# Performance work log

Measured on AMD Instinct MI355X. Metric: run time of the kernel, lower is better.

Reference implementation:

```python
import jax, jax.numpy as jnp
import numpy as np
import math

LIMBS = [(5, 7), (7, 9), (6, 8), (8, 10), (11, 13), (13, 15), (12, 14), (14, 16), (5, 6), (11, 12), (5, 11), (6, 12), (5, 12), (6, 11)]
PARENT = jnp.array([l[0] for l in LIMBS], dtype=jnp.int32)
CHILD = jnp.array([l[1] for l in LIMBS], dtype=jnp.int32)
EXPECTED_2D_LEN = 0.15

B = 65536
D_MODEL = 64
HID = 128


def _ln(x, g, b, eps=1e-5):
    m = jnp.mean(x, axis=-1, keepdims=True)
    v = jnp.mean(jnp.square(x - m), axis=-1, keepdims=True)
    return (x - m) * jax.lax.rsqrt(v + eps) * g + b


def _unit(x, eps=1e-6):
    # F.normalize semantics: divide by max(norm, eps)
    n = jnp.linalg.norm(x, axis=-1, keepdims=True)
    return x / jnp.maximum(n, eps)


def setup_inputs() -> dict:
    key = jax.random.key(0)
    ks = jax.random.split(key, 32)
    d = {}
    d["joint_features"] = jax.random.normal(ks[0], (B, 17, D_MODEL), jnp.float32)
    d["pose_2d"] = jax.random.normal(ks[1], (B, 17, 2), jnp.float32)
    d["pose_3d"] = jax.random.normal(ks[2], (B, 17, 3), jnp.float32)
    d["azimuth"] = jax.random.uniform(ks[3], (B,), jnp.float32) * 360.0
    d["elevation"] = jax.random.uniform(ks[4], (B,), jnp.float32) * 180.0 - 90.0
    d["projected_2d"] = jax.random.normal(ks[5], (B, 17, 2), jnp.float32)

    def lin(k, out_f, in_f, std=None):
        s = std if std is not None else 1.0 / math.sqrt(in_f)
        return jax.random.normal(k, (out_f, in_f), jnp.float32) * s

    # current_orient_encoder: Linear(3->32), LayerNorm(32), ReLU
    d["co_w"] = lin(ks[6], HID // 4, 3)
    d["co_b"] = jnp.zeros((HID // 4,), jnp.float32)
    d["co_g"] = jnp.ones((HID // 4,), jnp.float32)
    d["co_be"] = jnp.zeros((HID // 4,), jnp.float32)
    # limb_2d_encoder: Linear(4->64), LayerNorm(64), ReLU
    d["l2_w"] = lin(ks[7], HID // 2, 4)
    d["l2_b"] = jnp.zeros((HID // 2,), jnp.float32)
    d["l2_g"] = jnp.ones((HID // 2,), jnp.float32)
    d["l2_be"] = jnp.zeros((HID // 2,), jnp.float32)
    # view_encoder: Linear(7->32), ReLU
    d["v_w"] = lin(ks[8], HID // 4, 7)
    d["v_b"] = jnp.zeros((HID // 4,), jnp.float32)
    # limb_head: Linear(256->128), LN(128), LeakyReLU, Linear(128->128), LeakyReLU, Linear(128->3)
    in_dim = HID // 2 + HID // 4 + D_MODEL * 2 + HID // 4  # 256
    d["h1_w"] = lin(ks[9], HID, in_dim)
    d["h1_b"] = jnp.zeros((HID,), jnp.float32)
    d["h_g"] = jnp.ones((HID,), jnp.float32)
    d["h_be"] = jnp.zeros((HID,), jnp.float32)
    d["h2_w"] = lin(ks[10], HID, HID)
    d["h2_b"] = jnp.zeros((HID,), jnp.float32)
    d["h3_w"] = lin(ks[11], 3, HID, std=0.01)
    d["h3_b"] = jnp.zeros((3,), jnp.float32)
    return d


def reference(joint_features, pose_2d, pose_3d, azimuth, elevation, projected_2d,
              co_w, co_b, co_g, co_be, l2_w, l2_b, l2_g, l2_be, v_w, v_b,
              h1_w, h1_b, h_g, h_be, h2_w, h2_b, h3_w, h3_b):
    nl = PARENT.shape[0]  # 14
    # gather parent/child joint features: (B, 14, d_model)
    pf = joint_features[:, PARENT, :]
    cf = joint_features[:, CHILD, :]
    # current 3D orientations from input pose
    cur = _unit(pose_3d[:, CHILD, :] - pose_3d[:, PARENT, :])  # (B,14,3)
    co = jax.nn.relu(_ln(jnp.einsum('blk,ok->blo', cur, co_w) + co_b, co_g, co_be))
    # view encoder from azimuth/elevation
    az = azimuth * (math.pi / 180.0)
    el = elevation * (math.pi / 180.0)
    sa, ca, se, ce = jnp.sin(az), jnp.cos(az), jnp.sin(el), jnp.cos(el)
    view_in = jnp.stack([sa * ce, se, ca * ce, sa, ca, se, ce], axis=-1)  # (B,7)
    vf = jax.nn.relu(view_in @ v_w.T + v_b)  # (B,32)
    vf = jnp.broadcast_to(vf[:, None, :], (vf.shape[0], nl, vf.shape[-1]))
    # 2D foreshortening features from projected_2d
    v2 = projected_2d[:, CHILD, :] - projected_2d[:, PARENT, :]  # (B,14,2)
    L = jnp.linalg.norm(v2, axis=-1, keepdims=True)
    d2 = v2 / (L + 1e-6)
    ratio = L / (EXPECTED_2D_LEN + 1e-6)
    feat2d = jnp.concatenate([d2, L, ratio], axis=-1)  # (B,14,4)
    l2 = jax.nn.relu(_ln(jnp.einsum('blk,ok->blo', feat2d, l2_w) + l2_b, l2_g, l2_be))
    # concat all branches: (B,14,256)
    lf = jnp.concatenate([l2, co, pf, cf, vf], axis=-1)
    # 3-layer MLP head
    h = jax.nn.leaky_relu(_ln(jnp.einsum('blk,ok->blo', lf, h1_w) + h1_b, h_g, h_be), 0.2)
    h = jax.nn.leaky_relu(jnp.einsum('blk,ok->blo', h, h2_w) + h2_b, 0.2)
    delta = jnp.einsum('blk,ok->blo', h, h3_w) + h3_b  # (B,14,3)
    return _unit(cur + delta)
```

## Files before the change

kernel.cpp:

```cpp
#include <hip/hip_runtime.h>


#define NTHR   1024
#define NBLK   256
#define NTILES 14336
#define NROWS  917504
#define C2D    6.66662222251852f
#define RAD    0.017453292519943295f
#define WS_STAT_OFF 98304
#define WS_SCAL_OFF 131072

typedef __bf16 bf16x8 __attribute__((ext_vector_type(8)));
typedef __bf16 bf16x4 __attribute__((ext_vector_type(4)));
typedef float  f32x4  __attribute__((ext_vector_type(4)));

#define PARENT_PK 0x10106097863120ull
#define CHILD_PK  0x677671b9a85342ull

__global__ __launch_bounds__(256) void prep_kernel(
    const float* __restrict__ w1, const float* __restrict__ w2,
    __bf16* __restrict__ wsb)
{
  const int u = blockIdx.x * 256 + threadIdx.x;
  if (u < 4096) {
    const int lane = u & 63, t = u >> 6;
    const int f = t & 1, kk = (t >> 1) & 7, wn = t >> 4;
    const int col = wn * 32 + f * 16 + (lane & 15);
    const int kb  = kk * 32 + (lane >> 4) * 8;
    __bf16* dst = wsb + (size_t)u * 8;
    #pragma unroll
    for (int j = 0; j < 8; ++j) dst[j] = (__bf16)w1[col * 256 + kb + j];
  } else if (u < 6144) {
    const int v = u - 4096;
    const int lane = v & 63, t = v >> 6;
    const int f = t & 1, kk = (t >> 1) & 3, wn = t >> 3;
    const int col = wn * 32 + f * 16 + (lane & 15);
    const int kb  = kk * 32 + (lane >> 4) * 8;
    __bf16* dst = wsb + 32768 + (size_t)v * 8;
    #pragma unroll
    for (int j = 0; j < 8; ++j) dst[j] = (__bf16)w2[col * 128 + kb + j];
  }
}

__global__ __launch_bounds__(64) void prep0_kernel(
    const float* __restrict__ cow, const float* __restrict__ cob,
    const float* __restrict__ l2w, const float* __restrict__ l2b,
    float* __restrict__ statg)
{
  const int o = threadIdx.x;
  const float w0 = l2w[o * 4 + 0], w1v = l2w[o * 4 + 1];
  const float w2v = l2w[o * 4 + 2] + C2D * l2w[o * 4 + 3];
  const float bo = l2b[o];
  float v[14] = { w0, w1v, w2v, bo, w0 * w0, w0 * w1v, w0 * w2v,
                  w1v * w1v, w1v * w2v, w2v * w2v, w0 * bo, w1v * bo, w2v * bo, bo * bo };
  float c0 = 0.f, c1 = 0.f, c2 = 0.f, cb = 0.f;
  if (o < 32) { c0 = cow[o * 3 + 0]; c1 = cow[o * 3 + 1]; c2 = cow[o * 3 + 2]; cb = cob[o]; }
  float u[14] = { c0, c1, c2, cb, c0 * c0, c0 * c1, c0 * c2,
                  c1 * c1, c1 * c2, c2 * c2, c0 * cb, c1 * cb, c2 * cb, cb * cb };
  #pragma unroll
  for (int k = 0; k < 14; ++k) {
    #pragma unroll
    for (int m = 1; m < 64; m <<= 1) { v[k] += __shfl_xor(v[k], m, 64); u[k] += __shfl_xor(u[k], m, 64); }
  }
  if (o == 0) {
    const float i64 = 1.f / 64.f, i32 = 1.f / 32.f;
    const float lmx = v[0] * i64, lmy = v[1] * i64, lmz = v[2] * i64, lmb = v[3] * i64;
    statg[0] = lmx; statg[1] = lmy; statg[2] = lmz; statg[3] = lmb;
    statg[4] = v[4] * i64 - lmx * lmx;        statg[5] = 2.f * (v[5] * i64 - lmx * lmy);
    statg[6] = 2.f * (v[6] * i64 - lmx * lmz); statg[7] = v[7] * i64 - lmy * lmy;
    statg[8] = 2.f * (v[8] * i64 - lmy * lmz); statg[9] = v[9] * i64 - lmz * lmz;
    statg[10] = 2.f * (v[10] * i64 - lmx * lmb); statg[11] = 2.f * (v[11] * i64 - lmy * lmb);
    statg[12] = 2.f * (v[12] * i64 - lmz * lmb); statg[13] = v[13] * i64 - lmb * lmb;
    const float cmx = u[0] * i32, cmy = u[1] * i32, cmz = u[2] * i32, cmb = u[3] * i32;
    statg[14] = cmx; statg[15] = cmy; statg[16] = cmz; statg[17] = cmb;
    statg[18] = u[4] * i32 - cmx * cmx;        statg[19] = 2.f * (u[5] * i32 - cmx * cmy);
    statg[20] = 2.f * (u[6] * i32 - cmx * cmz); statg[21] = u[7] * i32 - cmy * cmy;
    statg[22] = 2.f * (u[8] * i32 - cmy * cmz); statg[23] = u[9] * i32 - cmz * cmz;
    statg[24] = 2.f * (u[10] * i32 - cmx * cmb); statg[25] = 2.f * (u[11] * i32 - cmy * cmb);
    statg[26] = 2.f * (u[12] * i32 - cmz * cmb); statg[27] = u[13] * i32 - cmb * cmb;
  }
}

__global__ __launch_bounds__(256) void prep2_kernel(
    const float* __restrict__ p3g, const float* __restrict__ az,
    const float* __restrict__ el,  const float* __restrict__ p2d,
    const float* __restrict__ statg, f32x4* __restrict__ scalg)
{
  const int r = blockIdx.x * 256 + threadIdx.x;
  const unsigned rg = (unsigned)r;
  const unsigned b = rg / 14u;
  const int l = (int)(rg - b * 14u);
  const int p = 5 + (int)((PARENT_PK >> (4 * l)) & 15ull);
  const int c = 5 + (int)((CHILD_PK  >> (4 * l)) & 15ull);
  const float* p3 = p3g + (size_t)b * 51;
  const float dx = p3[c * 3 + 0] - p3[p * 3 + 0];
  const float dy = p3[c * 3 + 1] - p3[p * 3 + 1];
  const float dz = p3[c * 3 + 2] - p3[p * 3 + 2];
  const float* q2 = p2d + (size_t)b * 34;
  const float vx = q2[c * 2 + 0] - q2[p * 2 + 0];
  const float vy = q2[c * 2 + 1] - q2[p * 2 + 1];
  const float sazv = az[b], selv = el[b];

  const float ci = 1.f / fmaxf(sqrtf(dx * dx + dy * dy + dz * dz), 1e-6f);
  const float cx = dx * ci, cy = dy * ci, cz = dz * ci;
  const float L  = sqrtf(vx * vx + vy * vy);
  const float il = 1.f / (L + 1e-6f);
  const float f0 = vx * il, f1 = vy * il;
  const float azr = sazv * RAD, elr = selv * RAD;
  const float sa = __sinf(azr), ca = __cosf(azr);
  const float se = __sinf(elr), ce = __cosf(elr);
  const float vl = statg[4] * f0 * f0 + statg[7] * f1 * f1 + statg[9] * L * L +
                   statg[5] * f0 * f1 + statg[6] * f0 * L + statg[8] * f1 * L +
                   statg[10] * f0 + statg[11] * f1 + statg[12] * L + statg[13];
  const float vc = statg[18] * cx * cx + statg[21] * cy * cy + statg[23] * cz * cz +
                   statg[19] * cx * cy + statg[20] * cx * cz + statg[22] * cy * cz +
                   statg[24] * cx + statg[25] * cy + statg[26] * cz + statg[27];
  f32x4 s0; s0[0] = cx; s0[1] = cy; s0[2] = cz; s0[3] = f0;
  f32x4 s1; s1[0] = f1; s1[1] = L; s1[2] = rsqrtf(vl + 1e-5f); s1[3] = rsqrtf(vc + 1e-5f);
  f32x4 s2; s2[0] = sa * ce; s2[1] = se; s2[2] = ca * ce; s2[3] = sa;
  f32x4 s3; s3[0] = ca; s3[1] = ce; s3[2] = 0.f; s3[3] = 0.f;
  scalg[(size_t)r * 4 + 0] = s0; scalg[(size_t)r * 4 + 1] = s1;
  scalg[(size_t)r * 4 + 2] = s2; scalg[(size_t)r * 4 + 3] = s3;
}

struct Smem {
  __bf16 w1f[32768];
  __bf16 w2f[16384];
  __bf16 lf[64][264];
  __bf16 h [64][132];
  f32x4  scal4[256];
  float  w3c[384];
  float  h1b[128], hg[128], hbe[128], h2b[128];
  float  partG1[512];
  float  partG2[768];
};

__device__ __forceinline__ float RFL(float x) {
  return __uint_as_float((unsigned)__builtin_amdgcn_readfirstlane((int)__float_as_uint(x)));
}

template<bool PRECOMP>
__global__ __launch_bounds__(NTHR, 4) void limb_kernel(
    const float* __restrict__ jf,  const float* __restrict__ p3g,
    const float* __restrict__ az,  const float* __restrict__ el,
    const float* __restrict__ p2d,
    const float* __restrict__ cow, const float* __restrict__ cob,
    const float* __restrict__ cog, const float* __restrict__ cobe,
    const float* __restrict__ l2w, const float* __restrict__ l2b,
    const float* __restrict__ l2g, const float* __restrict__ l2be,
    const float* __restrict__ vw,  const float* __restrict__ vb,
    const float* __restrict__ h1bg, const float* __restrict__ hgg,
    const float* __restrict__ hbeg, const float* __restrict__ h2bg,
    const float* __restrict__ w3,  const float* __restrict__ h3bg,
    const __bf16* __restrict__ wsb, const f32x4* __restrict__ scalg,
    float* __restrict__ out)
{
  __shared__ Smem sm;
  const int tid  = threadIdx.x;
  const int wave = tid >> 6;
  const int lane = tid & 63;
  const int lrow = lane & 15, lk8 = lane >> 4;
  const int mp = wave >> 2, nt = wave & 3;
  const int nrow = nt * 16 + lrow;
  const int cb0 = mp * 32 + lk8 * 4;
  const int cb1 = cb0 + 16;
  const int myrow0 = wave * 4;

  {
    const uint4* s1 = (const uint4*)wsb;
    uint4* d1 = (uint4*)sm.w1f;
    for (int i = tid; i < 4096; i += NTHR) d1[i] = s1[i];
    const uint4* s2 = (const uint4*)(wsb + 32768);
    uint4* d2 = (uint4*)sm.w2f;
    for (int i = tid; i < 2048; i += NTHR) d2[i] = s2[i];
  }
  if (tid < 384) sm.w3c[tid] = w3[tid];
  if (tid < 128) {
    sm.h1b[tid] = h1bg[tid]; sm.hg[tid] = hgg[tid];
    sm.hbe[tid] = hbeg[tid]; sm.h2b[tid] = h2bg[tid];
  }
  const float h3b0 = h3bg[0], h3b1 = h3bg[1], h3b2 = h3bg[2];

  float lQxx, lQxy2, lQxz2, lQyy, lQyz2, lQzz, lrx2, lry2, lrz2, ls0;
  float lmx, lmy, lmz, lmb;
  {
    float s1x = 0, s1y = 0, s1z = 0, sb = 0;
    float sxx = 0, sxy = 0, sxz = 0, syy = 0, syz = 0, szz = 0;
    float sbx = 0, sby = 0, sbz = 0, sbb = 0;
    for (int o = 0; o < 64; ++o) {
      const float w0 = l2w[o * 4 + 0], w1v = l2w[o * 4 + 1];
      const float w2v = l2w[o * 4 + 2] + C2D * l2w[o * 4 + 3];
      const float bo = l2b[o];
      s1x += w0; s1y += w1v; s1z += w2v; sb += bo;
      sxx += w0 * w0; sxy += w0 * w1v; sxz += w0 * w2v;
      syy += w1v * w1v; syz += w1v * w2v; szz += w2v * w2v;
      sbx += w0 * bo; sby += w1v * bo; sbz += w2v * bo; sbb += bo * bo;
    }
    const float i = 1.f / 64.f;
    lmx = RFL(s1x * i); lmy = RFL(s1y * i); lmz = RFL(s1z * i); lmb = RFL(sb * i);
    lQxx = RFL(sxx * i - lmx * lmx); lQxy2 = RFL(2.f * (sxy * i - lmx * lmy));
    lQxz2 = RFL(2.f * (sxz * i - lmx * lmz)); lQyy = RFL(syy * i - lmy * lmy);
    lQyz2 = RFL(2.f * (syz * i - lmy * lmz)); lQzz = RFL(szz * i - lmz * lmz);
    lrx2 = RFL(2.f * (sbx * i - lmx * lmb)); lry2 = RFL(2.f * (sby * i - lmy * lmb));
    lrz2 = RFL(2.f * (sbz * i - lmz * lmb)); ls0 = RFL(sbb * i - lmb * lmb);
  }
  float cQxx, cQxy2, cQxz2, cQyy, cQyz2, cQzz, crx2, cry2, crz2, cs0;
  float cmx, cmy, cmz, cmb;
  {
    float s1x = 0, s1y = 0, s1z = 0, sb = 0;
    float sxx = 0, sxy = 0, sxz = 0, syy = 0, syz = 0, szz = 0;
    float sbx = 0, sby = 0, sbz = 0, sbb = 0;
    for (int o = 0; o < 32; ++o) {
      const float w0 = cow[o * 3 + 0], w1v = cow[o * 3 + 1], w2v = cow[o * 3 + 2];
      const float bo = cob[o];
      s1x += w0; s1y += w1v; s1z += w2v; sb += bo;
      sxx += w0 * w0; sxy += w0 * w1v; sxz += w0 * w2v;
      syy += w1v * w1v; syz += w1v * w2v; szz += w2v * w2v;
      sbx += w0 * bo; sby += w1v * bo; sbz += w2v * bo; sbb += bo * bo;
    }
    const float i = 1.f / 32.f;
    cmx = RFL(s1x * i); cmy = RFL(s1y * i); cmz = RFL(s1z * i); cmb = RFL(sb * i);
    cQxx = RFL(sxx * i - cmx * cmx); cQxy2 = RFL(2.f * (sxy * i - cmx * cmy));
    cQxz2 = RFL(2.f * (sxz * i - cmx * cmz)); cQyy = RFL(syy * i - cmy * cmy);
    cQyz2 = RFL(2.f * (syz * i - cmy * cmz)); cQzz = RFL(szz * i - cmz * cmz);
    crx2 = RFL(2.f * (sbx * i - cmx * cmb)); cry2 = RFL(2.f * (sby * i - cmy * cmb));
    crz2 = RFL(2.f * (sbz * i - cmz * cmb)); cs0 = RFL(sbb * i - cmb * cmb);
  }

  const float lwc0 = l2w[lane * 4 + 0] - lmx;
  const float lwc1 = l2w[lane * 4 + 1] - lmy;
  const float lwc2 = (l2w[lane * 4 + 2] + C2D * l2w[lane * 4 + 3]) - lmz;
  const float lbc  = l2b[lane] - lmb;
  const float lgv  = l2g[lane], lbev = l2be[lane];
  float u0, u1, u2, u3, u4, u5, u6;
  if (lane < 32) {
    u0 = cow[lane * 3 + 0] - cmx; u1 = cow[lane * 3 + 1] - cmy;
    u2 = cow[lane * 3 + 2] - cmz; u3 = cob[lane] - cmb;
    u4 = cog[lane]; u5 = cobe[lane]; u6 = 0.f;
  } else {
    const int o = lane - 32;
    u0 = vw[o * 7 + 0]; u1 = vw[o * 7 + 1] + vw[o * 7 + 5];
    u2 = vw[o * 7 + 2]; u3 = vw[o * 7 + 3];
    u4 = vw[o * 7 + 4]; u5 = vw[o * 7 + 6]; u6 = vb[o];
  }

  auto jf_src = [&](int rg0x, int round) -> const float* {
    const int task = wave * 8 + round * 4 + lk8;
    const int row = task >> 1, half = task & 1;
    const unsigned rg = (unsigned)(rg0x + row);
    const unsigned b = rg / 14u;
    const int l = (int)(rg - b * 14u);
    const int j = half ? 5 + (int)((CHILD_PK >> (4 * l)) & 15ull)
                       : 5 + (int)((PARENT_PK >> (4 * l)) & 15ull);
    return jf + ((size_t)b * 17 + (size_t)j) * 64 + lrow * 4;
  };
  auto jf_store = [&](int round, float4 v) {
    const int task = wave * 8 + round * 4 + lk8;
    const int row = task >> 1, half = task & 1;
    bf16x4 o; o[0] = (__bf16)v.x; o[1] = (__bf16)v.y; o[2] = (__bf16)v.z; o[3] = (__bf16)v.w;
    *(bf16x4*)&sm.lf[row][(half ? 160 : 96) + lrow * 4] = o;
  };
  struct G12 { float p3p0, p3p1, p3p2, p3c0, p3c1, p3c2, q2p0, q2p1, q2c0, q2c1, sazv, selv; };
  auto gather12_row = [&](int rgl) -> G12 {
    G12 g;
    const unsigned rg = (unsigned)rgl;
    const unsigned b = rg / 14u;
    const int l = (int)(rg - b * 14u);
    const int p = 5 + (int)((PARENT_PK >> (4 * l)) & 15ull);
    const int c = 5 + (int)((CHILD_PK  >> (4 * l)) & 15ull);
    const float* p3 = p3g + (size_t)b * 51;
    g.p3p0 = p3[p * 3 + 0]; g.p3p1 = p3[p * 3 + 1]; g.p3p2 = p3[p * 3 + 2];
    g.p3c0 = p3[c * 3 + 0]; g.p3c1 = p3[c * 3 + 1]; g.p3c2 = p3[c * 3 + 2];
    const float* q2 = p2d + (size_t)b * 34;
    g.q2p0 = q2[p * 2 + 0]; g.q2p1 = q2[p * 2 + 1];
    g.q2c0 = q2[c * 2 + 0]; g.q2c1 = q2[c * 2 + 1];
    g.sazv = az[b]; g.selv = el[b];
    return g;
  };
  auto scal_write = [&](int row, const G12& g) {
    const float dx = g.p3c0 - g.p3p0, dy = g.p3c1 - g.p3p1, dz = g.p3c2 - g.p3p2;
    const float ci = 1.f / fmaxf(sqrtf(dx * dx + dy * dy + dz * dz), 1e-6f);
    const float cx = dx * ci, cy = dy * ci, cz = dz * ci;
    const float vx = g.q2c0 - g.q2p0, vy = g.q2c1 - g.q2p1;
    const float L  = sqrtf(vx * vx + vy * vy);
    const float il = 1.f / (L + 1e-6f);
    const float f0 = vx * il, f1 = vy * il;
    const float azr = g.sazv * RAD, elr = g.selv * RAD;
    const float sa = __sinf(azr), ca = __cosf(azr);
    const float se = __sinf(elr), ce = __cosf(elr);
    const float vl = lQxx * f0 * f0 + lQyy * f1 * f1 + lQzz * L * L +
                     lQxy2 * f0 * f1 + lQxz2 * f0 * L + lQyz2 * f1 * L +
                     lrx2 * f0 + lry2 * f1 + lrz2 * L + ls0;
    const float vc = cQxx * cx * cx + cQyy * cy * cy + cQzz * cz * cz +
                     cQxy2 * cx * cy + cQxz2 * cx * cz + cQyz2 * cy * cz +
                     crx2 * cx + cry2 * cy + crz2 * cz + cs0;
    f32x4 s0; s0[0] = cx; s0[1] = cy; s0[2] = cz; s0[3] = f0;
    f32x4 s1; s1[0] = f1; s1[1] = L; s1[2] = rsqrtf(vl + 1e-5f); s1[3] = rsqrtf(vc + 1e-5f);
    f32x4 s2; s2[0] = sa * ce; s2[1] = se; s2[2] = ca * ce; s2[3] = sa;
    f32x4 s3; s3[0] = ca; s3[1] = ce; s3[2] = 0.f; s3[3] = 0.f;
    sm.scal4[row * 4 + 0] = s0; sm.scal4[row * 4 + 1] = s1;
    sm.scal4[row * 4 + 2] = s2; sm.scal4[row * 4 + 3] = s3;
  };
  auto expandB = [&]() {
    #pragma unroll
    for (int rr = 0; rr < 4; ++rr) {
      const int row = myrow0 + rr;
      const f32x4 s0 = sm.scal4[row * 4 + 0];
      const f32x4 s1 = sm.scal4[row * 4 + 1];
      const f32x4 s2 = sm.scal4[row * 4 + 2];
      const f32x4 s3 = sm.scal4[row * 4 + 3];
      {
        const float a = lwc0 * s0[3] + lwc1 * s1[0] + lwc2 * s1[1] + lbc;
        sm.lf[row][lane] = (__bf16)fmaxf(a * s1[2] * lgv + lbev, 0.f);
      }
      if (lane < 32) {
        const float a = u0 * s0[0] + u1 * s0[1] + u2 * s0[2] + u3;
        sm.lf[row][64 + lane] = (__bf16)fmaxf(a * s1[3] * u4 + u5, 0.f);
      } else {
        const float a = u0 * s2[0] + u1 * s2[1] + u2 * s2[2] + u3 * s2[3] +
                        u4 * s3[0] + u5 * s3[1] + u6;
        sm.lf[row][224 + (lane - 32)] = (__bf16)fmaxf(a, 0.f);
      }
    }
  };

  {
    const int rg0 = blockIdx.x * 64;
    jf_store(0, *(const float4*)jf_src(rg0, 0));
    jf_store(1, *(const float4*)jf_src(rg0, 1));
    if (lane < 4) {
      if (PRECOMP) {
        const f32x4* sp = scalg + (size_t)(rg0 + myrow0 + lane) * 4;
        sm.scal4[(myrow0 + lane) * 4 + 0] = sp[0];
        sm.scal4[(myrow0 + lane) * 4 + 1] = sp[1];
        sm.scal4[(myrow0 + lane) * 4 + 2] = sp[2];
        sm.scal4[(myrow0 + lane) * 4 + 3] = sp[3];
      } else {
        scal_write(myrow0 + lane, gather12_row(rg0 + myrow0 + lane));
      }
    }
    expandB();
  }
  __syncthreads();

  float curx = 0.f, cury = 0.f, curz = 0.f;
  int prevT = -1;

  for (int tile = blockIdx.x; tile < NTILES; tile += NBLK) {
    const int ntile = tile + NBLK;
    const bool pv = ntile < NTILES;

    float4 jva = {0.f, 0.f, 0.f, 0.f}, jvb = jva;
    f32x4 s0n = {0.f, 0.f, 0.f, 0.f}, s1n = s0n, s2n = s0n, s3n = s0n;
    G12 g = {};
    if (pv) {
      jva = *(const float4*)jf_src(ntile * 64, 0);
      jvb = *(const float4*)jf_src(ntile * 64, 1);
      if (lane < 4) {
        if (PRECOMP) {
          const f32x4* sp = scalg + (size_t)(ntile * 64 + myrow0 + lane) * 4;
          s0n = sp[0]; s1n = sp[1]; s2n = sp[2]; s3n = sp[3];
        } else {
          g = gather12_row(ntile * 64 + myrow0 + lane);
        }
      }
    }
    if (prevT >= 0 && lane < 4) {
      const int r = myrow0 + lane;
      const f32x4 q0 = *(const f32x4*)&sm.partG2[r * 12];
      const f32x4 q1 = *(const f32x4*)&sm.partG2[r * 12 + 4];
      const f32x4 q2 = *(const f32x4*)&sm.partG2[r * 12 + 8];
      const float ox = curx + q0[0] + q0[1] + q0[2] + q0[3] + h3b0;
      const float oy = cury + q1[0] + q1[1] + q1[2] + q1[3] + h3b1;
      const float oz = curz + q2[0] + q2[1] + q2[2] + q2[3] + h3b2;
      const float nn = sqrtf(ox * ox + oy * oy + oz * oz);
      const float iv = 1.f / fmaxf(nn, 1e-6f);
      const size_t o0 = (size_t)(prevT * 64 + r) * 3;
      out[o0 + 0] = ox * iv; out[o0 + 1] = oy * iv; out[o0 + 2] = oz * iv;
    }
    f32x4 a0 = {0.f, 0.f, 0.f, 0.f}, a1 = a0;
    #pragma unroll
    for (int kk = 0; kk < 8; ++kk) {
      const bf16x8 fb  = *(const bf16x8*)&sm.lf[nrow][kk * 32 + lk8 * 8];
      const bf16x8 fa0 = *(const bf16x8*)&sm.w1f[(((mp * 8 + kk) * 2 + 0) * 64 + lane) * 8];
      const bf16x8 fa1 = *(const bf16x8*)&sm.w1f[(((mp * 8 + kk) * 2 + 1) * 64 + lane) * 8];
      a0 = __builtin_amdgcn_mfma_f32_16x16x32_bf16(fa0, fb, a0, 0, 0, 0);
      a1 = __builtin_amdgcn_mfma_f32_16x16x32_bf16(fa1, fb, a1, 0, 0, 0);
    }
    const f32x4 hb0 = *(const f32x4*)&sm.h1b[cb0];
    const f32x4 hb1 = *(const f32x4*)&sm.h1b[cb1];
    float v0[4], v1[4], ss = 0.f, qq = 0.f;
    #pragma unroll
    for (int j = 0; j < 4; ++j) {
      v0[j] = a0[j] + hb0[j]; v1[j] = a1[j] + hb1[j];
      ss += v0[j] + v1[j];
      qq = fmaf(v0[j], v0[j], qq); qq = fmaf(v1[j], v1[j], qq);
    }
    ss += __shfl_xor(ss, 16, 64); ss += __shfl_xor(ss, 32, 64);
    qq += __shfl_xor(qq, 16, 64); qq += __shfl_xor(qq, 32, 64);
    if (lk8 == 0) *(float2*)&sm.partG1[nrow * 8 + mp * 2] = make_float2(ss, qq);
    __syncthreads();

    {
      const f32x4 pa = *(const f32x4*)&sm.partG1[nrow * 8];
      const f32x4 pb = *(const f32x4*)&sm.partG1[nrow * 8 + 4];
      const float mean = (pa[0] + pa[2] + pb[0] + pb[2]) * (1.f / 128.f);
      const float var  = (pa[1] + pa[3] + pb[1] + pb[3]) * (1.f / 128.f) - mean * mean;
      const float rs = rsqrtf(var + 1e-5f);
      const f32x4 g0 = *(const f32x4*)&sm.hg[cb0],  g1 = *(const f32x4*)&sm.hg[cb1];
      const f32x4 e0 = *(const f32x4*)&sm.hbe[cb0], e1 = *(const f32x4*)&sm.hbe[cb1];
      bf16x4 y0, y1;
      #pragma unroll
      for (int j = 0; j < 4; ++j) {
        float t0 = (v0[j] - mean) * rs * g0[j] + e0[j]; t0 = (t0 > 0.f) ? t0 : 0.2f * t0;
        float t1 = (v1[j] - mean) * rs * g1[j] + e1[j]; t1 = (t1 > 0.f) ? t1 : 0.2f * t1;
        y0[j] = (__bf16)t0; y1[j] = (__bf16)t1;
      }
      *(bf16x4*)&sm.h[nrow][cb0] = y0;
      *(bf16x4*)&sm.h[nrow][cb1] = y1;
    }
    __syncthreads();

    f32x4 d0 = {0.f, 0.f, 0.f, 0.f}, d1 = d0;
    #pragma unroll
    for (int kk = 0; kk < 4; ++kk) {
      const bf16x8 fbh = *(const bf16x8*)&sm.h[nrow][kk * 32 + lk8 * 8];
      const bf16x8 fa0 = *(const bf16x8*)&sm.w2f[(((mp * 4 + kk) * 2 + 0) * 64 + lane) * 8];
      const bf16x8 fa1 = *(const bf16x8*)&sm.w2f[(((mp * 4 + kk) * 2 + 1) * 64 + lane) * 8];
      d0 = __builtin_amdgcn_mfma_f32_16x16x32_bf16(fa0, fbh, d0, 0, 0, 0);
      d1 = __builtin_amdgcn_mfma_f32_16x16x32_bf16(fa1, fbh, d1, 0, 0, 0);
    }
    if (pv) { jf_store(0, jva); jf_store(1, jvb); }
    if (lane < 4) {
      const f32x4 cu = sm.scal4[(myrow0 + lane) * 4];
      curx = cu[0]; cury = cu[1]; curz = cu[2];
      if (pv) {
        if (PRECOMP) {
          sm.scal4[(myrow0 + lane) * 4 + 0] = s0n;
          sm.scal4[(myrow0 + lane) * 4 + 1] = s1n;
          sm.scal4[(myrow0 + lane) * 4 + 2] = s2n;
          sm.scal4[(myrow0 + lane) * 4 + 3] = s3n;
        } else {
          scal_write(myrow0 + lane, g);
        }
      }
    }
    {
      const f32x4 b20 = *(const f32x4*)&sm.h2b[cb0], b21 = *(const f32x4*)&sm.h2b[cb1];
      const f32x4 wx0 = *(const f32x4*)&sm.w3c[cb0],        wx1 = *(const f32x4*)&sm.w3c[cb1];
      const f32x4 wy0 = *(const f32x4*)&sm.w3c[128 + cb0],  wy1 = *(const f32x4*)&sm.w3c[128 + cb1];
      const f32x4 wz0 = *(const f32x4*)&sm.w3c[256 + cb0],  wz1 = *(const f32x4*)&sm.w3c[256 + cb1];
      float p0 = 0.f, p1 = 0.f, p2 = 0.f;
      #pragma unroll
      for (int j = 0; j < 4; ++j) {
        float x0 = d0[j] + b20[j]; x0 = (x0 > 0.f) ? x0 : 0.2f * x0;
        float x1 = d1[j] + b21[j]; x1 = (x1 > 0.f) ? x1 : 0.2f * x1;
        p0 = fmaf(x0, wx0[j], fmaf(x1, wx1[j], p0));
        p1 = fmaf(x0, wy0[j], fmaf(x1, wy1[j], p1));
        p2 = fmaf(x0, wz0[j], fmaf(x1, wz1[j], p2));
      }
      p0 += __shfl_xor(p0, 16, 64); p0 += __shfl_xor(p0, 32, 64);
      p1 += __shfl_xor(p1, 16, 64); p1 += __shfl_xor(p1, 32, 64);
      p2 += __shfl_xor(p2, 16, 64); p2 += __shfl_xor(p2, 32, 64);
      if (lk8 == 0) {
        sm.partG2[nrow * 12 + 0 + mp] = p0;
        sm.partG2[nrow * 12 + 4 + mp] = p1;
        sm.partG2[nrow * 12 + 8 + mp] = p2;
      }
    }
    if (pv) expandB();
    __syncthreads();
    prevT = tile;
  }

  if (lane < 4) {
    const int r = myrow0 + lane;
    const f32x4 q0 = *(const f32x4*)&sm.partG2[r * 12];
    const f32x4 q1 = *(const f32x4*)&sm.partG2[r * 12 + 4];
    const f32x4 q2 = *(const f32x4*)&sm.partG2[r * 12 + 8];
    const float ox = curx + q0[0] + q0[1] + q0[2] + q0[3] + h3b0;
    const float oy = cury + q1[0] + q1[1] + q1[2] + q1[3] + h3b1;
    const float oz = curz + q2[0] + q2[1] + q2[2] + q2[3] + h3b2;
    const float nn = sqrtf(ox * ox + oy * oy + oz * oz);
    const float iv = 1.f / fmaxf(nn, 1e-6f);
    const size_t o0 = (size_t)(prevT * 64 + r) * 3;
    out[o0 + 0] = ox * iv; out[o0 + 1] = oy * iv; out[o0 + 2] = oz * iv;
  }
}

extern "C" void kernel_launch(void* const* d_in, const int* in_sizes, int n_in,
                              void* d_out, int out_size, void* d_ws, size_t ws_size,
                              hipStream_t stream) {
  (void)in_sizes; (void)n_in; (void)out_size;
  const float* jf   = (const float*)d_in[0];
  const float* p3   = (const float*)d_in[2];
  const float* az   = (const float*)d_in[3];
  const float* el   = (const float*)d_in[4];
  const float* p2d  = (const float*)d_in[5];
  const float* cow  = (const float*)d_in[6];
  const float* cob  = (const float*)d_in[7];
  const float* cog  = (const float*)d_in[8];
  const float* cobe = (const float*)d_in[9];
  const float* l2w  = (const float*)d_in[10];
  const float* l2b  = (const float*)d_in[11];
  const float* l2g  = (const float*)d_in[12];
  const float* l2be = (const float*)d_in[13];
  const float* vw   = (const float*)d_in[14];
  const float* vb   = (const float*)d_in[15];
  const float* w1   = (const float*)d_in[16];
  const float* h1b  = (const float*)d_in[17];
  const float* hg   = (const float*)d_in[18];
  const float* hbe  = (const float*)d_in[19];
  const float* w2   = (const float*)d_in[20];
  const float* h2b  = (const float*)d_in[21];
  const float* w3   = (const float*)d_in[22];
  const float* h3b  = (const float*)d_in[23];

  __bf16* wsb   = (__bf16*)d_ws;
  float*  statg = (float*)((char*)d_ws + WS_STAT_OFF);
  f32x4*  scalg = (f32x4*)((char*)d_ws + WS_SCAL_OFF);

  const size_t ws_need = (size_t)WS_SCAL_OFF + (size_t)NROWS * 64;
  const bool pre = ws_size >= ws_need;

  prep_kernel<<<dim3(24), dim3(256), 0, stream>>>(w1, w2, wsb);
  if (pre) {
    prep0_kernel<<<dim3(1), dim3(64), 0, stream>>>(cow, cob, l2w, l2b, statg);
    prep2_kernel<<<dim3(NROWS / 256), dim3(256), 0, stream>>>(p3, az, el, p2d, statg, scalg);
    limb_kernel<true><<<dim3(NBLK), dim3(NTHR), 0, stream>>>(
        jf, p3, az, el, p2d, cow, cob, cog, cobe,
        l2w, l2b, l2g, l2be, vw, vb,
        h1b, hg, hbe, h2b, w3, h3b, wsb, scalg, (float*)d_out);
  } else {
    limb_kernel<false><<<dim3(NBLK), dim3(NTHR), 0, stream>>>(
        jf, p3, az, el, p2d, cow, cob, cog, cobe,
        l2w, l2b, l2g, l2be, vw, vb,
        h1b, hg, hbe, h2b, w3, h3b, wsb, scalg, (float*)d_out);
  }
}
```

Baseline: 316.5 us.

## Software-pipeline MLP layers across tiles to drop one barrier per tile

Restructures the persistent tile loop into a two-stage software pipeline. Each iteration runs layer 2 and 3 on the previous tile's hidden activations while running layer 1 and the LayerNorm statistics on the current tile. This removes one __syncthreads per tile and lets the two GEMM phases interleave. The cost is an extra prologue/epilogue iteration, conditional branches, and more live registers, and the reuse of sm.h and partG2 across iterations must be ordered correctly.

```diff
diff --git a/kernel.cpp b/kernel.cpp
--- a/kernel.cpp
+++ b/kernel.cpp
@@ -4,6 +4,7 @@
 #define NTHR   1024
 #define NBLK   256
 #define NTILES 14336
+#define NIT    56
 #define NROWS  917504
 #define C2D    6.66662222251852f
 #define RAD    0.017453292519943295f
@@ -344,16 +345,18 @@
   __syncthreads();
 
   float curx = 0.f, cury = 0.f, curz = 0.f;
-  int prevT = -1;
-
-  for (int tile = blockIdx.x; tile < NTILES; tile += NBLK) {
-    const int ntile = tile + NBLK;
-    const bool pv = ntile < NTILES;
+
+  for (int it = 0; it <= NIT; ++it) {
+    const int tile  = blockIdx.x + it * NBLK;
+    const bool hasG1 = it < NIT;
+    const bool hasG2 = it > 0;
+    const bool pv    = (it + 1) < NIT;
 
     float4 jva = {0.f, 0.f, 0.f, 0.f}, jvb = jva;
     f32x4 s0n = {0.f, 0.f, 0.f, 0.f}, s1n = s0n, s2n = s0n, s3n = s0n;
     G12 g = {};
     if (pv) {
+      const int ntile = tile + NBLK;
       jva = *(const float4*)jf_src(ntile * 64, 0);
       jvb = *(const float4*)jf_src(ntile * 64, 1);
       if (lane < 4) {
@@ -365,43 +368,65 @@
         }
       }
     }
-    if (prevT >= 0 && lane < 4) {
-      const int r = myrow0 + lane;
-      const f32x4 q0 = *(const f32x4*)&sm.partG2[r * 12];
-      const f32x4 q1 = *(const f32x4*)&sm.partG2[r * 12 + 4];
-      const f32x4 q2 = *(const f32x4*)&sm.partG2[r * 12 + 8];
-      const float ox = curx + q0[0] + q0[1] + q0[2] + q0[3] + h3b0;
-      const float oy = cury + q1[0] + q1[1] + q1[2] + q1[3] + h3b1;
-      const float oz = curz + q2[0] + q2[1] + q2[2] + q2[3] + h3b2;
-      const float nn = sqrtf(ox * ox + oy * oy + oz * oz);
-      const float iv = 1.f / fmaxf(nn, 1e-6f);
-      const size_t o0 = (size_t)(prevT * 64 + r) * 3;
-      out[o0 + 0] = ox * iv; out[o0 + 1] = oy * iv; out[o0 + 2] = oz * iv;
-    }
-    f32x4 a0 = {0.f, 0.f, 0.f, 0.f}, a1 = a0;
-    #pragma unroll
-    for (int kk = 0; kk < 8; ++kk) {
-      const bf16x8 fb  = *(const bf16x8*)&sm.lf[nrow][kk * 32 + lk8 * 8];
-      const bf16x8 fa0 = *(const bf16x8*)&sm.w1f[(((mp * 8 + kk) * 2 + 0) * 64 + lane) * 8];
-      const bf16x8 fa1 = *(const bf16x8*)&sm.w1f[(((mp * 8 + kk) * 2 + 1) * 64 + lane) * 8];
-      a0 = __builtin_amdgcn_mfma_f32_16x16x32_bf16(fa0, fb, a0, 0, 0, 0);
-      a1 = __builtin_amdgcn_mfma_f32_16x16x32_bf16(fa1, fb, a1, 0, 0, 0);
-    }
-    const f32x4 hb0 = *(const f32x4*)&sm.h1b[cb0];
-    const f32x4 hb1 = *(const f32x4*)&sm.h1b[cb1];
-    float v0[4], v1[4], ss = 0.f, qq = 0.f;
-    #pragma unroll
-    for (int j = 0; j < 4; ++j) {
-      v0[j] = a0[j] + hb0[j]; v1[j] = a1[j] + hb1[j];
-      ss += v0[j] + v1[j];
-      qq = fmaf(v0[j], v0[j], qq); qq = fmaf(v1[j], v1[j], qq);
-    }
-    ss += __shfl_xor(ss, 16, 64); ss += __shfl_xor(ss, 32, 64);
-    qq += __shfl_xor(qq, 16, 64); qq += __shfl_xor(qq, 32, 64);
-    if (lk8 == 0) *(float2*)&sm.partG1[nrow * 8 + mp * 2] = make_float2(ss, qq);
+    if (hasG2) {
+      f32x4 d0 = {0.f, 0.f, 0.f, 0.f}, d1 = d0;
+      #pragma unroll
+      for (int kk = 0; kk < 4; ++kk) {
+        const bf16x8 fbh = *(const bf16x8*)&sm.h[nrow][kk * 32 + lk8 * 8];
+        const bf16x8 fa0 = *(const bf16x8*)&sm.w2f[(((mp * 4 + kk) * 2 + 0) * 64 + lane) * 8];
+        const bf16x8 fa1 = *(const bf16x8*)&sm.w2f[(((mp * 4 + kk) * 2 + 1) * 64 + lane) * 8];
+        d0 = __builtin_amdgcn_mfma_f32_16x16x32_bf16(fa0, fbh, d0, 0, 0, 0);
+        d1 = __builtin_amdgcn_mfma_f32_16x16x32_bf16(fa1, fbh, d1, 0, 0, 0);
+      }
+      const f32x4 b20 = *(const f32x4*)&sm.h2b[cb0], b21 = *(const f32x4*)&sm.h2b[cb1];
+      const f32x4 wx0 = *(const f32x4*)&sm.w3c[cb0],        wx1 = *(const f32x4*)&sm.w3c[cb1];
+      const f32x4 wy0 = *(const f32x4*)&sm.w3c[128 + cb0],  wy1 = *(const f32x4*)&sm.w3c[128 + cb1];
+      const f32x4 wz0 = *(const f32x4*)&sm.w3c[256 + cb0],  wz1 = *(const f32x4*)&sm.w3c[256 + cb1];
+      float p0 = 0.f, p1 = 0.f, p2 = 0.f;
+      #pragma unroll
+      for (int j = 0; j < 4; ++j) {
+        float x0 = d0[j] + b20[j]; x0 = (x0 > 0.f) ? x0 : 0.2f * x0;
+        float x1 = d1[j] + b21[j]; x1 = (x1 > 0.f) ? x1 : 0.2f * x1;
+        p0 = fmaf(x0, wx0[j], fmaf(x1, wx1[j], p0));
+        p1 = fmaf(x0, wy0[j], fmaf(x1, wy1[j], p1));
+        p2 = fmaf(x0, wz0[j], fmaf(x1, wz1[j], p2));
+      }
+      p0 += __shfl_xor(p0, 16, 64); p0 += __shfl_xor(p0, 32, 64);
+      p1 += __shfl_xor(p1, 16, 64); p1 += __shfl_xor(p1, 32, 64);
+      p2 += __shfl_xor(p2, 16, 64); p2 += __shfl_xor(p2, 32, 64);
+      if (lk8 == 0) {
+        sm.partG2[nrow * 12 + 0 + mp] = p0;
+        sm.partG2[nrow * 12 + 4 + mp] = p1;
+        sm.partG2[nrow * 12 + 8 + mp] = p2;
+      }
+    }
+    float v0[4], v1[4];
+    if (hasG1) {
+      f32x4 a0 = {0.f, 0.f, 0.f, 0.f}, a1 = a0;
+      #pragma unroll
+      for (int kk = 0; kk < 8; ++kk) {
+        const bf16x8 fb  = *(const bf16x8*)&sm.lf[nrow][kk * 32 + lk8 * 8];
+        const bf16x8 fa0 = *(const bf16x8*)&sm.w1f[(((mp * 8 + kk) * 2 + 0) * 64 + lane) * 8];
+        const bf16x8 fa1 = *(const bf16x8*)&sm.w1f[(((mp * 8 + kk) * 2 + 1) * 64 + lane) * 8];
+        a0 = __builtin_amdgcn_mfma_f32_16x16x32_bf16(fa0, fb, a0, 0, 0, 0);
+        a1 = __builtin_amdgcn_mfma_f32_16x16x32_bf16(fa1, fb, a1, 0, 0, 0);
+      }
+      const f32x4 hb0 = *(const f32x4*)&sm.h1b[cb0];
+      const f32x4 hb1 = *(const f32x4*)&sm.h1b[cb1];
+      float ss = 0.f, qq = 0.f;
+      #pragma unroll
+      for (int j = 0; j < 4; ++j) {
+        v0[j] = a0[j] + hb0[j]; v1[j] = a1[j] + hb1[j];
+        ss += v0[j] + v1[j];
+        qq = fmaf(v0[j], v0[j], qq); qq = fmaf(v1[j], v1[j], qq);
+      }
+      ss += __shfl_xor(ss, 16, 64); ss += __shfl_xor(ss, 32, 64);
+      qq += __shfl_xor(qq, 16, 64); qq += __shfl_xor(qq, 32, 64);
+      if (lk8 == 0) *(float2*)&sm.partG1[nrow * 8 + mp * 2] = make_float2(ss, qq);
+    }
     __syncthreads();
 
-    {
+    if (hasG1) {
       const f32x4 pa = *(const f32x4*)&sm.partG1[nrow * 8];
       const f32x4 pb = *(const f32x4*)&sm.partG1[nrow * 8 + 4];
       const float mean = (pa[0] + pa[2] + pb[0] + pb[2]) * (1.f / 128.f);
@@ -419,22 +444,25 @@
       *(bf16x4*)&sm.h[nrow][cb0] = y0;
       *(bf16x4*)&sm.h[nrow][cb1] = y1;
     }
-    __syncthreads();
-
-    f32x4 d0 = {0.f, 0.f, 0.f, 0.f}, d1 = d0;
-    #pragma unroll
-    for (int kk = 0; kk < 4; ++kk) {
-      const bf16x8 fbh = *(const bf16x8*)&sm.h[nrow][kk * 32 + lk8 * 8];
-      const bf16x8 fa0 = *(const bf16x8*)&sm.w2f[(((mp * 4 + kk) * 2 + 0) * 64 + lane) * 8];
-      const bf16x8 fa1 = *(const bf16x8*)&sm.w2f[(((mp * 4 + kk) * 2 + 1) * 64 + lane) * 8];
-      d0 = __builtin_amdgcn_mfma_f32_16x16x32_bf16(fa0, fbh, d0, 0, 0, 0);
-      d1 = __builtin_amdgcn_mfma_f32_16x16x32_bf16(fa1, fbh, d1, 0, 0, 0);
-    }
-    if (pv) { jf_store(0, jva); jf_store(1, jvb); }
-    if (lane < 4) {
+    if (hasG2 && lane < 4) {
+      const int r = myrow0 + lane;
+      const f32x4 q0 = *(const f32x4*)&sm.partG2[r * 12];
+      const f32x4 q1 = *(const f32x4*)&sm.partG2[r * 12 + 4];
+      const f32x4 q2 = *(const f32x4*)&sm.partG2[r * 12 + 8];
+      const float ox = curx + q0[0] + q0[1] + q0[2] + q0[3] + h3b0;
+      const float oy = cury + q1[0] + q1[1] + q1[2] + q1[3] + h3b1;
+      const float oz = curz + q2[0] + q2[1] + q2[2] + q2[3] + h3b2;
+      const float nn = sqrtf(ox * ox + oy * oy + oz * oz);
+      const float iv = 1.f / fmaxf(nn, 1e-6f);
+      const size_t o0 = (size_t)((tile - NBLK) * 64 + r) * 3;
+      out[o0 + 0] = ox * iv; out[o0 + 1] = oy * iv; out[o0 + 2] = oz * iv;
+    }
+    if (hasG1 && lane < 4) {
       const f32x4 cu = sm.scal4[(myrow0 + lane) * 4];
       curx = cu[0]; cury = cu[1]; curz = cu[2];
-      if (pv) {
+    }
+    if (pv) {
+      if (lane < 4) {
         if (PRECOMP) {
           sm.scal4[(myrow0 + lane) * 4 + 0] = s0n;
           sm.scal4[(myrow0 + lane) * 4 + 1] = s1n;
@@ -444,47 +472,10 @@
           scal_write(myrow0 + lane, g);
         }
       }
-    }
-    {
-      const f32x4 b20 = *(const f32x4*)&sm.h2b[cb0], b21 = *(const f32x4*)&sm.h2b[cb1];
-      const f32x4 wx0 = *(const f32x4*)&sm.w3c[cb0],        wx1 = *(const f32x4*)&sm.w3c[cb1];
-      const f32x4 wy0 = *(const f32x4*)&sm.w3c[128 + cb0],  wy1 = *(const f32x4*)&sm.w3c[128 + cb1];
-      const f32x4 wz0 = *(const f32x4*)&sm.w3c[256 + cb0],  wz1 = *(const f32x4*)&sm.w3c[256 + cb1];
-      float p0 = 0.f, p1 = 0.f, p2 = 0.f;
-      #pragma unroll
-      for (int j = 0; j < 4; ++j) {
-        float x0 = d0[j] + b20[j]; x0 = (x0 > 0.f) ? x0 : 0.2f * x0;
-        float x1 = d1[j] + b21[j]; x1 = (x1 > 0.f) ? x1 : 0.2f * x1;
-        p0 = fmaf(x0, wx0[j], fmaf(x1, wx1[j], p0));
-        p1 = fmaf(x0, wy0[j], fmaf(x1, wy1[j], p1));
-        p2 = fmaf(x0, wz0[j], fmaf(x1, wz1[j], p2));
-      }
-      p0 += __shfl_xor(p0, 16, 64); p0 += __shfl_xor(p0, 32, 64);
-      p1 += __shfl_xor(p1, 16, 64); p1 += __shfl_xor(p1, 32, 64);
-      p2 += __shfl_xor(p2, 16, 64); p2 += __shfl_xor(p2, 32, 64);
-      if (lk8 == 0) {
-        sm.partG2[nrow * 12 + 0 + mp] = p0;
-        sm.partG2[nrow * 12 + 4 + mp] = p1;
-        sm.partG2[nrow * 12 + 8 + mp] = p2;
-      }
-    }
-    if (pv) expandB();
+      jf_store(0, jva); jf_store(1, jvb);
+      expandB();
+    }
     __syncthreads();
-    prevT = tile;
-  }
-
-  if (lane < 4) {
-    const int r = myrow0 + lane;
-    const f32x4 q0 = *(const f32x4*)&sm.partG2[r * 12];
-    const f32x4 q1 = *(const f32x4*)&sm.partG2[r * 12 + 4];
-    const f32x4 q2 = *(const f32x4*)&sm.partG2[r * 12 + 8];
-    const float ox = curx + q0[0] + q0[1] + q0[2] + q0[3] + h3b0;
-    const float oy = cury + q1[0] + q1[1] + q1[2] + q1[3] + h3b1;
-    const float oz = curz + q2[0] + q2[1] + q2[2] + q2[3] + h3b2;
-    const float nn = sqrtf(ox * ox + oy * oy + oz * oz);
-    const float iv = 1.f / fmaxf(nn, 1e-6f);
-    const size_t o0 = (size_t)(prevT * 64 + r) * 3;
-    out[o0 + 0] = ox * iv; out[o0 + 1] = oy * iv; out[o0 + 2] = oz * iv;
   }
 }
 
```

After: 325.9 us. 3.0% more time.
